# Performance work log

Hardware: AMD Instinct MI355X
Metric: run time of the kernel (lower is better)

The kernel has to match this reference:

```python
import jax, jax.numpy as jnp
import numpy as np


def setup_inputs() -> dict:
    key = jax.random.key(0)
    k1, k2 = jax.random.split(key)
    B, S, D, K = 32, 8192, 256, 64
    attention = jax.random.normal(k1, (B, S), dtype=jnp.float32)
    context = jax.random.normal(k2, (B, S, D), dtype=jnp.float32)
    return {"attention": attention, "context": context, "K": K}


def reference(attention, context, K):
    # per-batch top-K over attention scores, then gather context rows
    _, idx = jax.lax.top_k(attention, K)          # idx: [B, K]
    # gather: out[b, k, :] = context[b, idx[b, k], :]
    out = jnp.take_along_axis(context, idx[:, :, None], axis=1)  # [B, K, D]
    return out
```

## Files before the change

kernel.cpp:

```cpp
#include <hip/hip_runtime.h>


constexpr int BATCH   = 32;
constexpr int S       = 8192;
constexpr int D       = 256;
constexpr int K       = 64;
constexpr int THREADS = 256;
constexpr int NBINS   = 16384;
constexpr int CAP     = 256;

__device__ __forceinline__ unsigned int mono_key(float f) {
    unsigned int u = __float_as_uint(f);
    return (u & 0x80000000u) ? ~u : (u | 0x80000000u);
}
__device__ __forceinline__ unsigned long long umax64(unsigned long long a, unsigned long long b) {
    return a > b ? a : b;
}
__device__ __forceinline__ unsigned long long umin64(unsigned long long a, unsigned long long b) {
    return a < b ? a : b;
}

__global__ __launch_bounds__(THREADS) void topk_gather_kernel(
    const float* __restrict__ att,
    const float* __restrict__ ctx,
    float* __restrict__ out)
{
    const int b    = blockIdx.x;
    const int tid  = threadIdx.x;
    const int lane = tid & 63;
    const int wid  = tid >> 6;

    __shared__ unsigned int       hist[NBINS];
    __shared__ unsigned long long s_cand[CAP];
    __shared__ unsigned long long s_sort[THREADS];
    __shared__ unsigned int       s_wsum[THREADS / 64];
    __shared__ unsigned int       s_cnt, s_chunk, s_above, s_T;
    __shared__ int                s_idx[K];

    for (int i = tid; i < NBINS; i += THREADS) hist[i] = 0u;
    if (tid == 0) s_cnt = 0u;
    __syncthreads();

    const float4* arow4 = (const float4*)(att + (size_t)b * S);
    float4 f[8];
#pragma unroll
    for (int j = 0; j < 8; ++j) {
        f[j] = arow4[tid + j * THREADS];
        atomicAdd(&hist[mono_key(f[j].x) >> 18], 1u);
        atomicAdd(&hist[mono_key(f[j].y) >> 18], 1u);
        atomicAdd(&hist[mono_key(f[j].z) >> 18], 1u);
        atomicAdd(&hist[mono_key(f[j].w) >> 18], 1u);
    }
    __syncthreads();

    unsigned int mypart = 0;
    {
        const uint4* h4 = (const uint4*)hist;
        int cb = tid * 16;
#pragma unroll
        for (int j = 0; j < 16; ++j) {
            uint4 u = h4[cb + ((j + tid) & 15)];
            mypart += u.x + u.y + u.z + u.w;
        }
    }

    unsigned int suf = mypart;
#pragma unroll
    for (int off = 1; off < 64; off <<= 1) {
        unsigned int o = __shfl_down(suf, off, 64);
        if (lane + off < 64) suf += o;
    }
    if (lane == 0) s_wsum[wid] = suf;
    __syncthreads();
    for (int w = wid + 1; w < THREADS / 64; ++w) suf += s_wsum[w];
    unsigned int sufnext = suf - mypart;

    if (suf >= (unsigned)K && sufnext < (unsigned)K) {
        s_chunk = (unsigned)tid;
        s_above = sufnext;
    }
    __syncthreads();

    if (wid == 0) {
        int base = (int)s_chunk * 64;
        unsigned int above = s_above;
        unsigned int cf = hist[base + lane];
#pragma unroll
        for (int off = 1; off < 64; off <<= 1) {
            unsigned int o = __shfl_down(cf, off, 64);
            if (lane + off < 64) cf += o;
        }
        unsigned long long mask = __ballot(above + cf >= (unsigned)K);
        if (lane == 0) s_T = (unsigned)(base + 63 - __clzll(mask));
    }
    __syncthreads();
    const unsigned int T = s_T;

#pragma unroll
    for (int j = 0; j < 8; ++j) {
        int base = 4 * (tid + j * THREADS);
        float v[4] = {f[j].x, f[j].y, f[j].z, f[j].w};
#pragma unroll
        for (int c = 0; c < 4; ++c) {
            unsigned int k32 = mono_key(v[c]);
            if ((k32 >> 18) >= T) {
                unsigned p = atomicAdd(&s_cnt, 1u);
                if (p < (unsigned)CAP)
                    s_cand[p] = ((unsigned long long)k32 << 32) |
                                (unsigned int)(S - 1 - (base + c));
            }
        }
    }
    __syncthreads();

    unsigned int C = s_cnt;
    unsigned long long key = (tid < (int)C) ? s_cand[tid] : 0ull;

#pragma unroll
    for (int k = 2; k <= THREADS; k <<= 1) {
        for (int j = k >> 1; j > 0; j >>= 1) {
            unsigned long long other;
            if (j < 64) {
                other = __shfl_xor(key, j, 64);
            } else {
                __syncthreads();
                s_sort[tid] = key;
                __syncthreads();
                other = s_sort[tid ^ j];
            }
            bool low     = (tid & j) == 0;
            bool descSeg = (tid & k) == 0;
            key = (low == descSeg) ? umax64(key, other) : umin64(key, other);
        }
    }

    if (tid < K) s_idx[tid] = S - 1 - (int)(unsigned int)(key & 0xFFFFFFFFull);
    __syncthreads();

    const float4* ctx4 = (const float4*)(ctx + (size_t)b * S * D);
    float4*       out4 = (float4*)(out + (size_t)b * K * D);
    constexpr int ROW4 = D / 4;
#pragma unroll
    for (int e = tid; e < K * ROW4; e += THREADS) {
        int k = e >> 6;
        int c = e & (ROW4 - 1);
        out4[e] = ctx4[(size_t)s_idx[k] * ROW4 + c];
    }
}

extern "C" void kernel_launch(void* const* d_in, const int* in_sizes, int n_in,
                              void* d_out, int out_size, void* d_ws, size_t ws_size,
                              hipStream_t stream) {
    const float* att = (const float*)d_in[0];
    const float* ctx = (const float*)d_in[1];
    float* out = (float*)d_out;

    topk_gather_kernel<<<BATCH, THREADS, 0, stream>>>(att, ctx, out);
}
```

Before: 314.8 us.

## Split top-k selection and row gather into separate kernels

The fused kernel is split so that the per-batch top-k selection writes its indices to workspace memory. A second, widely launched kernel then gathers the context rows, one float4 per thread. The aim is to spread the gather across many blocks instead of the 32 per-batch blocks, to improve memory-level parallelism. The cost is an extra kernel launch and a global round-trip for the index array.

Result: no change. 308.8 us (-1.9%).

```diff
diff --git a/kernel.cpp b/kernel.cpp
--- a/kernel.cpp
+++ b/kernel.cpp
@@ -20,10 +20,9 @@
     return a < b ? a : b;
 }
 
-__global__ __launch_bounds__(THREADS) void topk_gather_kernel(
+__global__ __launch_bounds__(THREADS) void topk_select_kernel(
     const float* __restrict__ att,
-    const float* __restrict__ ctx,
-    float* __restrict__ out)
+    int* __restrict__ idx_out)
 {
     const int b    = blockIdx.x;
     const int tid  = threadIdx.x;
@@ -35,7 +34,6 @@
     __shared__ unsigned long long s_sort[THREADS];
     __shared__ unsigned int       s_wsum[THREADS / 64];
     __shared__ unsigned int       s_cnt, s_chunk, s_above, s_T;
-    __shared__ int                s_idx[K];
 
     for (int i = tid; i < NBINS; i += THREADS) hist[i] = 0u;
     if (tid == 0) s_cnt = 0u;
@@ -134,18 +132,27 @@
         }
     }
 
-    if (tid < K) s_idx[tid] = S - 1 - (int)(unsigned int)(key & 0xFFFFFFFFull);
-    __syncthreads();
+    if (tid < K)
+        idx_out[b * K + tid] = S - 1 - (int)(unsigned int)(key & 0xFFFFFFFFull);
+}
 
-    const float4* ctx4 = (const float4*)(ctx + (size_t)b * S * D);
-    float4*       out4 = (float4*)(out + (size_t)b * K * D);
-    constexpr int ROW4 = D / 4;
-#pragma unroll
-    for (int e = tid; e < K * ROW4; e += THREADS) {
-        int k = e >> 6;
-        int c = e & (ROW4 - 1);
-        out4[e] = ctx4[(size_t)s_idx[k] * ROW4 + c];
-    }
+constexpr int ROW4     = D / 4;
+constexpr int GTHREADS = 256;
+constexpr int GBLOCKS  = BATCH * K * ROW4 / GTHREADS;
+
+__global__ __launch_bounds__(GTHREADS) void gather_kernel(
+    const float* __restrict__ ctx,
+    const int*   __restrict__ idx,
+    float*       __restrict__ out)
+{
+    const int e  = blockIdx.x * GTHREADS + threadIdx.x;
+    const int bk = e >> 6;
+    const int c  = e & (ROW4 - 1);
+    const int b  = bk >> 6;
+    const int row = idx[bk];
+
+    const float4* ctx4 = (const float4*)ctx;
+    ((float4*)out)[e] = ctx4[((size_t)b * S + row) * ROW4 + c];
 }
 
 extern "C" void kernel_launch(void* const* d_in, const int* in_sizes, int n_in,
@@ -154,6 +161,8 @@
     const float* att = (const float*)d_in[0];
     const float* ctx = (const float*)d_in[1];
     float* out = (float*)d_out;
+    int*   idx = (int*)d_ws;
 
-    topk_gather_kernel<<<BATCH, THREADS, 0, stream>>>(att, ctx, out);
+    topk_select_kernel<<<BATCH, THREADS, 0, stream>>>(att, idx);
+    gather_kernel<<<GBLOCKS, GTHREADS, 0, stream>>>(ctx, idx, out);
 }
```
